# Performance work log

Hardware: AMD Instinct MI355X
Metric: run time of the kernel (lower is better)

The kernel has to match this reference:

```python
import jax, jax.numpy as jnp
import numpy as np

N_NODES = 100000


def _graph_conv(x, W, b, src, dst, n_nodes):
    # DGL GraphConv, norm='both':
    #   h = x * out_deg(src)^{-1/2}; h = h @ W; agg = scatter_sum over dst;
    #   out = agg * in_deg(dst)^{-1/2} + b
    ones = jnp.ones(src.shape, dtype=x.dtype)
    out_deg = jax.ops.segment_sum(ones, src, num_segments=n_nodes)
    in_deg = jax.ops.segment_sum(ones, dst, num_segments=n_nodes)
    norm_src = jax.lax.rsqrt(jnp.maximum(out_deg, 1.0))  # [N]
    norm_dst = jax.lax.rsqrt(jnp.maximum(in_deg, 1.0))   # [N]
    h = (x * norm_src[:, None]) @ W                      # [N, hid]
    msgs = h[src]                                        # [E, hid] gather
    agg = jax.ops.segment_sum(msgs, dst, num_segments=n_nodes)  # [N, hid]
    return jax.nn.relu(agg * norm_dst[:, None] + b)


def setup_inputs() -> dict:
    key = jax.random.key(0)
    k1, k2, k3, k4, k5 = jax.random.split(key, 5)
    n, e, d = N_NODES, 1600000, 128
    x = jax.random.normal(k1, (n, d), dtype=jnp.float32)
    src = jax.random.randint(k2, (e,), 0, n, dtype=jnp.int32)
    dst = jax.random.randint(k3, (e,), 0, n, dtype=jnp.int32)
    # Xavier-ish init for GraphConv weights, zero bias (DGL default)
    W1 = jax.random.normal(k4, (d, d), dtype=jnp.float32) / np.sqrt(d)
    W2 = jax.random.normal(k5, (d, d), dtype=jnp.float32) / np.sqrt(d)
    b1 = jnp.zeros((d,), dtype=jnp.float32)
    b2 = jnp.zeros((d,), dtype=jnp.float32)
    return {"x": x, "W1": W1, "b1": b1, "W2": W2, "b2": b2, "src": src, "dst": dst}


def reference(x, W1, b1, W2, b2, src, dst):
    h = _graph_conv(x, W1, b1, src, dst, N_NODES)
    h = _graph_conv(h, W2, b2, src, dst, N_NODES)
    return h
```

## Files before the change

kernel.cpp:

```cpp
#include <hip/hip_runtime.h>
#include <hip/hip_fp16.h>

#define HD 128
#define CHUNK 8192
#define MAXNB 512

typedef _Float16 f16x8 __attribute__((ext_vector_type(8)));
typedef float f32x4 __attribute__((ext_vector_type(4)));

__global__ __launch_bounds__(256) void hist_coarse(const int* __restrict__ dst,
                                                   unsigned int* __restrict__ gHist,
                                                   int NB, int NC, int E) {
    __shared__ unsigned int hist[MAXNB];
    for (int b = threadIdx.x; b < NB; b += 256) hist[b] = 0;
    __syncthreads();
    int base = blockIdx.x * CHUNK;
    int e0 = base + 4 * threadIdx.x;
#pragma unroll
    for (int it = 0; it < CHUNK / 1024; ++it, e0 += 1024) {
        if (e0 + 3 < E) {
            int4 d4 = *(const int4*)(dst + e0);
            atomicAdd(&hist[d4.x >> 8], 1u);
            atomicAdd(&hist[d4.y >> 8], 1u);
            atomicAdd(&hist[d4.z >> 8], 1u);
            atomicAdd(&hist[d4.w >> 8], 1u);
        } else {
            for (int j = 0; j < 4; ++j)
                if (e0 + j < E) atomicAdd(&hist[dst[e0 + j] >> 8], 1u);
        }
    }
    __syncthreads();
    for (int b = threadIdx.x; b < NB; b += 256)
        gHist[(size_t)b * NC + blockIdx.x] = hist[b];
}

__global__ __launch_bounds__(256) void make_norm_src(const unsigned int* __restrict__ cnt4s,
                                                     float* __restrict__ norm_src, int N) {
    int i = blockIdx.x * 256 + threadIdx.x;
    if (i < N) {
        float od = (float)(cnt4s[i] + cnt4s[N + i] + cnt4s[2 * N + i] + cnt4s[3 * N + i]);
        norm_src[i] = rsqrtf(od > 1.f ? od : 1.f);
    }
}

__global__ __launch_bounds__(256) void prep_w(const float* __restrict__ W1,
                                              const float* __restrict__ W2,
                                              _Float16* __restrict__ Wt) {
    const float* W = blockIdx.x ? W2 : W1;
    _Float16* T = Wt + (size_t)blockIdx.x * HD * HD;
    for (int i = threadIdx.x; i < HD * HD; i += 256) {
        int k = i >> 7, c = i & 127;
        T[c * HD + k] = (_Float16)W[i];
    }
}

__global__ __launch_bounds__(256) void scan_a(const unsigned int* __restrict__ cnt,
                                              unsigned int* __restrict__ excl,
                                              unsigned int* __restrict__ bsum, int n) {
    int i = blockIdx.x * 256 + threadIdx.x;
    unsigned int v = (i < n) ? cnt[i] : 0u;
    unsigned int x = v;
#pragma unroll
    for (int d = 1; d < 64; d <<= 1) {
        unsigned int y = __shfl_up(x, d, 64);
        if ((threadIdx.x & 63) >= d) x += y;
    }
    __shared__ unsigned int wsum[4];
    if ((threadIdx.x & 63) == 63) wsum[threadIdx.x >> 6] = x;
    __syncthreads();
    unsigned int woff = 0;
    for (int w = 0; w < (int)(threadIdx.x >> 6); ++w) woff += wsum[w];
    unsigned int incl = x + woff;
    if (i < n) excl[i] = incl - v;
    if (threadIdx.x == 255) bsum[blockIdx.x] = incl;
}

__global__ __launch_bounds__(1024) void scan_b(const unsigned int* __restrict__ bsum,
                                               unsigned int* __restrict__ boff, int nb) {
    int t = threadIdx.x;
    unsigned int v = (t < nb) ? bsum[t] : 0u;
    unsigned int x = v;
#pragma unroll
    for (int d = 1; d < 64; d <<= 1) {
        unsigned int y = __shfl_up(x, d, 64);
        if ((t & 63) >= d) x += y;
    }
    __shared__ unsigned int wsum[16];
    if ((t & 63) == 63) wsum[t >> 6] = x;
    __syncthreads();
    unsigned int woff = 0;
    for (int w = 0; w < (t >> 6); ++w) woff += wsum[w];
    unsigned int incl = x + woff;
    if (t < nb) boff[t] = incl - v;
}

__global__ __launch_bounds__(256) void scan_c(unsigned int* __restrict__ excl,
                                              const unsigned int* __restrict__ boff, int n) {
    int i = blockIdx.x * 256 + threadIdx.x;
    if (i < n) excl[i] += boff[blockIdx.x];
}

__global__ __launch_bounds__(256) void scatter_coarse(const int* __restrict__ src,
                                                      const int* __restrict__ dst,
                                                      const unsigned int* __restrict__ scanA,
                                                      unsigned int* __restrict__ packed,
                                                      unsigned int* __restrict__ cnt4s,
                                                      int N, int NB, int NC, int E) {
    __shared__ unsigned int curs[MAXNB];
    int chunk = blockIdx.x;
    for (int b = threadIdx.x; b < NB; b += 256)
        curs[b] = scanA[(size_t)b * NC + chunk];
    __syncthreads();
    int base = chunk * CHUNK;
    int e0 = base + 4 * threadIdx.x;
#pragma unroll
    for (int it = 0; it < CHUNK / 1024; ++it, e0 += 1024) {
        if (e0 + 3 < E) {
            int4 s4 = *(const int4*)(src + e0);
            int4 d4 = *(const int4*)(dst + e0);
            atomicAdd(&cnt4s[0 * N + s4.x], 1u);
            atomicAdd(&cnt4s[1 * N + s4.y], 1u);
            atomicAdd(&cnt4s[2 * N + s4.z], 1u);
            atomicAdd(&cnt4s[3 * N + s4.w], 1u);
            unsigned int p0 = atomicAdd(&curs[d4.x >> 8], 1u);
            unsigned int p1 = atomicAdd(&curs[d4.y >> 8], 1u);
            unsigned int p2 = atomicAdd(&curs[d4.z >> 8], 1u);
            unsigned int p3 = atomicAdd(&curs[d4.w >> 8], 1u);
            packed[p0] = ((unsigned int)(d4.x & 255) << 24) | (unsigned int)s4.x;
            packed[p1] = ((unsigned int)(d4.y & 255) << 24) | (unsigned int)s4.y;
            packed[p2] = ((unsigned int)(d4.z & 255) << 24) | (unsigned int)s4.z;
            packed[p3] = ((unsigned int)(d4.w & 255) << 24) | (unsigned int)s4.w;
        } else {
            for (int j = 0; j < 4; ++j)
                if (e0 + j < E) {
                    int d = dst[e0 + j], s = src[e0 + j];
                    atomicAdd(&cnt4s[j * N + s], 1u);
                    unsigned int pos = atomicAdd(&curs[d >> 8], 1u);
                    packed[pos] = ((unsigned int)(d & 255) << 24) | (unsigned int)s;
                }
        }
    }
}

__global__ __launch_bounds__(256) void fine_sort(const unsigned int* __restrict__ packed,
                                                 const unsigned int* __restrict__ scanA,
                                                 int* __restrict__ sorted_src,
                                                 unsigned int* __restrict__ offsets,
                                                 unsigned int* __restrict__ cntg,
                                                 float* __restrict__ normd,
                                                 int NB, int NC, int N, int E) {
    __shared__ unsigned int cnt[256];
    __shared__ unsigned int curs[256];
    __shared__ unsigned int wsum[4];
    int b = blockIdx.x;
    int t = threadIdx.x;
    unsigned int S = scanA[(size_t)b * NC];
    unsigned int T = (b + 1 < NB) ? scanA[(size_t)(b + 1) * NC] : (unsigned int)E;
    cnt[t] = 0;
    __syncthreads();
    for (unsigned int j = S + t; j < T; j += 256)
        atomicAdd(&cnt[packed[j] >> 24], 1u);
    __syncthreads();
    unsigned int v = cnt[t], x = v;
    int lane = t & 63;
#pragma unroll
    for (int d = 1; d < 64; d <<= 1) {
        unsigned int y = __shfl_up(x, d, 64);
        if (lane >= d) x += y;
    }
    if (lane == 63) wsum[t >> 6] = x;
    __syncthreads();
    unsigned int woff = 0;
    for (int w = 0; w < (t >> 6); ++w) woff += wsum[w];
    unsigned int ex = x - v + woff;
    curs[t] = ex;
    int node = b * 256 + t;
    if (node < N) {
        offsets[node] = S + ex;
        cntg[node] = v;
        float f = (float)v;
        normd[node] = rsqrtf(f > 1.f ? f : 1.f);
    }
    __syncthreads();
    for (unsigned int j = S + t; j < T; j += 256) {
        unsigned int p = packed[j];
        unsigned int pos = S + atomicAdd(&curs[p >> 24], 1u);
        sorted_src[pos] = (int)(p & 0xFFFFFFu);
    }
}

__global__ __launch_bounds__(256) void gemm_mfma_f32(const float* __restrict__ x,
                                                     const float* __restrict__ norm,
                                                     const _Float16* __restrict__ Wt,
                                                     _Float16* __restrict__ h, int n) {
    const int tid = threadIdx.x;
    const int w  = tid >> 6;
    const int l  = tid & 63;
    const int lg = l >> 4;
    const int li = l & 15;
    const int m  = blockIdx.x * 64 + w * 16 + li;

    f16x8 xf[4];
    if (m < n) {
        float nr = norm[m];
        const float* xrow = x + (size_t)m * HD + lg * 8;
#pragma unroll
        for (int kk = 0; kk < 4; ++kk) {
            float4 a = *(const float4*)(xrow + kk * 32);
            float4 b = *(const float4*)(xrow + kk * 32 + 4);
            f16x8 v;
            v[0] = (_Float16)(a.x * nr); v[1] = (_Float16)(a.y * nr);
            v[2] = (_Float16)(a.z * nr); v[3] = (_Float16)(a.w * nr);
            v[4] = (_Float16)(b.x * nr); v[5] = (_Float16)(b.y * nr);
            v[6] = (_Float16)(b.z * nr); v[7] = (_Float16)(b.w * nr);
            xf[kk] = v;
        }
    } else {
#pragma unroll
        for (int kk = 0; kk < 4; ++kk) xf[kk] = (f16x8){};
    }

    f32x4 acc[8];
#pragma unroll
    for (int t = 0; t < 8; ++t) acc[t] = (f32x4){0.f, 0.f, 0.f, 0.f};

#pragma unroll
    for (int t = 0; t < 8; ++t) {
        const _Float16* wrow = Wt + (size_t)(t * 16 + li) * HD + lg * 8;
#pragma unroll
        for (int kk = 0; kk < 4; ++kk) {
            f16x8 wf = *(const f16x8*)(wrow + kk * 32);
            acc[t] = __builtin_amdgcn_mfma_f32_16x16x32_f16(wf, xf[kk], acc[t], 0, 0, 0);
        }
    }

    if (m < n) {
        _Float16* hp = h + (size_t)m * HD + lg * 4;
#pragma unroll
        for (int t = 0; t < 8; ++t) {
            __half2 p0 = __floats2half2_rn(acc[t][0], acc[t][1]);
            __half2 p1 = __floats2half2_rn(acc[t][2], acc[t][3]);
            uint2 pk;
            pk.x = *(unsigned int*)&p0;
            pk.y = *(unsigned int*)&p1;
            *(uint2*)(hp + t * 16) = pk;
        }
    }
}

__global__ __launch_bounds__(256) void gemm_mfma(const _Float16* __restrict__ xh,
                                                 const _Float16* __restrict__ Wt,
                                                 _Float16* __restrict__ h, int n) {
    const int tid = threadIdx.x;
    const int w  = tid >> 6;
    const int l  = tid & 63;
    const int lg = l >> 4;
    const int li = l & 15;
    const int m  = blockIdx.x * 64 + w * 16 + li;

    const _Float16* xrow = xh + (size_t)m * HD + lg * 8;
    f16x8 xf[4];
#pragma unroll
    for (int kk = 0; kk < 4; ++kk)
        xf[kk] = *(const f16x8*)(xrow + kk * 32);

    f32x4 acc[8];
#pragma unroll
    for (int t = 0; t < 8; ++t) acc[t] = (f32x4){0.f, 0.f, 0.f, 0.f};

#pragma unroll
    for (int t = 0; t < 8; ++t) {
        const _Float16* wrow = Wt + (size_t)(t * 16 + li) * HD + lg * 8;
#pragma unroll
        for (int kk = 0; kk < 4; ++kk) {
            f16x8 wf = *(const f16x8*)(wrow + kk * 32);
            acc[t] = __builtin_amdgcn_mfma_f32_16x16x32_f16(wf, xf[kk], acc[t], 0, 0, 0);
        }
    }

    if (m < n) {
        _Float16* hp = h + (size_t)m * HD + lg * 4;
#pragma unroll
        for (int t = 0; t < 8; ++t) {
            __half2 p0 = __floats2half2_rn(acc[t][0], acc[t][1]);
            __half2 p1 = __floats2half2_rn(acc[t][2], acc[t][3]);
            uint2 pk;
            pk.x = *(unsigned int*)&p0;
            pk.y = *(unsigned int*)&p1;
            *(uint2*)(hp + t * 16) = pk;
        }
    }
}

template <bool MID>
__global__ __launch_bounds__(256) void aggregate_k(const __half* __restrict__ h,
                                                   const int* __restrict__ sorted_src,
                                                   const unsigned int* __restrict__ offsets,
                                                   const unsigned int* __restrict__ cnt,
                                                   const float* __restrict__ norm_dst,
                                                   const float* __restrict__ nsrc,
                                                   const float* __restrict__ bias,
                                                   float* __restrict__ outF,
                                                   __half* __restrict__ outH, int n) {
    int node = blockIdx.x * 4 + (int)(threadIdx.x >> 6);
    if (node >= n) return;
    int lane = threadIdx.x & 63;
    int g   = lane >> 4;
    int sub = lane & 15;

    unsigned int start = offsets[node];
    unsigned int deg   = cnt[node];
    const int* sp = sorted_src + start;
    const uint4* h4 = (const uint4*)h;

    float acc[8];
#pragma unroll
    for (int j = 0; j < 8; ++j) acc[j] = 0.f;

#define ACCUM(u)                                                                  \
    { float2 f;                                                                   \
      f = __half22float2(*(const __half2*)&(u).x); acc[0] += f.x; acc[1] += f.y;  \
      f = __half22float2(*(const __half2*)&(u).y); acc[2] += f.x; acc[3] += f.y;  \
      f = __half22float2(*(const __half2*)&(u).z); acc[4] += f.x; acc[5] += f.y;  \
      f = __half22float2(*(const __half2*)&(u).w); acc[6] += f.x; acc[7] += f.y; }

    unsigned int i = 0;
    for (; i + 16 <= deg; i += 16) {
        int s0 = sp[i + g];
        int s1 = sp[i + 4 + g];
        int s2 = sp[i + 8 + g];
        int s3 = sp[i + 12 + g];
        uint4 u0 = h4[(size_t)s0 * 16 + sub];
        uint4 u1 = h4[(size_t)s1 * 16 + sub];
        uint4 u2 = h4[(size_t)s2 * 16 + sub];
        uint4 u3 = h4[(size_t)s3 * 16 + sub];
        ACCUM(u0);
        ACCUM(u1);
        ACCUM(u2);
        ACCUM(u3);
    }
    for (; i < deg; i += 4) {
        if (i + g < deg) {
            int s = sp[i + g];
            uint4 u = h4[(size_t)s * 16 + sub];
            ACCUM(u);
        }
    }
#undef ACCUM

#pragma unroll
    for (int j = 0; j < 8; ++j) {
        acc[j] += __shfl_xor(acc[j], 16, 64);
        acc[j] += __shfl_xor(acc[j], 32, 64);
    }

    float nd = norm_dst[node];
    int col2 = sub * 4 + g;
    float2 bb = ((const float2*)bias)[col2];
    float vx = fmaxf(fmaf(acc[g * 2 + 0], nd, bb.x), 0.f);
    float vy = fmaxf(fmaf(acc[g * 2 + 1], nd, bb.y), 0.f);
    if (MID) {
        float ns = nsrc[node];
        __half2 p = __floats2half2_rn(vx * ns, vy * ns);
        ((__half2*)outH)[(size_t)node * 64 + col2] = p;
    } else {
        ((float2*)outF)[(size_t)node * 64 + col2] = make_float2(vx, vy);
    }
}

extern "C" void kernel_launch(void* const* d_in, const int* in_sizes, int n_in,
                              void* d_out, int out_size, void* d_ws, size_t ws_size,
                              hipStream_t stream) {
    const float* x   = (const float*)d_in[0];
    const float* W1  = (const float*)d_in[1];
    const float* b1  = (const float*)d_in[2];
    const float* W2  = (const float*)d_in[3];
    const float* b2  = (const float*)d_in[4];
    const int*   src = (const int*)d_in[5];
    const int*   dst = (const int*)d_in[6];

    const int N = in_sizes[0] / HD;
    const int E = in_sizes[5];
    float* out = (float*)d_out;

    const int NP = (N + 63) & ~63;
    const int NB = (N + 255) / 256;
    const int NC = (E + CHUNK - 1) / CHUNK;
    const int scanLen = NB * NC;
    const int nbS = (scanLen + 255) / 256;
    const int nbN = (N + 255) / 256;

    float*        norm_src = (float*)d_ws;
    float*        normd    = norm_src + N;
    unsigned int* cntg     = (unsigned int*)(normd + N);
    unsigned int* offsets  = cntg + N;
    unsigned int* cnt4s    = offsets + N;
    unsigned int* gHist    = cnt4s + 4 * N;
    unsigned int* scanA    = gHist + scanLen;
    unsigned int* bsum     = scanA + scanLen;
    unsigned int* boff     = bsum + 1024;
    unsigned int* packed   = boff + 1024;
    int*          sorted   = (int*)(packed + E);
    _Float16*     h        = (_Float16*)(sorted + E);
    _Float16*     xh       = h + (size_t)NP * HD;
    _Float16*     Wt       = xh + (size_t)NP * HD;

    hipMemsetAsync(cnt4s, 0, (size_t)4 * N * 4, stream);
    prep_w<<<2, 256, 0, stream>>>(W1, W2, Wt);
    hist_coarse<<<NC, 256, 0, stream>>>(dst, gHist, NB, NC, E);
    scan_a<<<nbS, 256, 0, stream>>>(gHist, scanA, bsum, scanLen);
    scan_b<<<1, 1024, 0, stream>>>(bsum, boff, nbS);
    scan_c<<<nbS, 256, 0, stream>>>(scanA, boff, scanLen);
    scatter_coarse<<<NC, 256, 0, stream>>>(src, dst, scanA, packed, cnt4s, N, NB, NC, E);
    make_norm_src<<<nbN, 256, 0, stream>>>(cnt4s, norm_src, N);
    fine_sort<<<NB, 256, 0, stream>>>(packed, scanA, sorted, offsets, cntg, normd, NB, NC, N, E);

    gemm_mfma_f32<<<NP / 64, 256, 0, stream>>>(x, norm_src, Wt, h, N);
    aggregate_k<true><<<(N + 3) / 4, 256, 0, stream>>>((const __half*)h, sorted, offsets, cntg,
                                                       normd, norm_src, b1, nullptr,
                                                       (__half*)xh, N);

    gemm_mfma<<<NP / 64, 256, 0, stream>>>(xh, Wt + HD * HD, h, N);
    aggregate_k<false><<<(N + 3) / 4, 256, 0, stream>>>((const __half*)h, sorted, offsets, cntg,
                                                        normd, nullptr, b2, out, nullptr, N);
}
```

Baseline: 352.0 us.

## Fold prep, scan fixup and norm kernels into neighbors; spread out-degree atomics

Merges the weight-transpose kernel into the coarse histogram launch as extra blocks, removes the scan_c fixup by adding block offsets on read in scatter and fine_sort, and computes norm_src inside fine_sort instead of a separate kernel. Out-degree counters are replicated eight ways instead of four to reduce global atomic contention. This cuts three kernel launches from the preprocessing chain. In exchange, the memset is larger and fine_sort must read eight count arrays.

```diff
diff --git a/kernel.cpp b/kernel.cpp
--- a/kernel.cpp
+++ b/kernel.cpp
@@ -8,9 +8,22 @@
 typedef _Float16 f16x8 __attribute__((ext_vector_type(8)));
 typedef float f32x4 __attribute__((ext_vector_type(4)));
 
-__global__ __launch_bounds__(256) void hist_coarse(const int* __restrict__ dst,
-                                                   unsigned int* __restrict__ gHist,
-                                                   int NB, int NC, int E) {
+__global__ __launch_bounds__(256) void hist_prep(const int* __restrict__ dst,
+                                                 unsigned int* __restrict__ gHist,
+                                                 const float* __restrict__ W1,
+                                                 const float* __restrict__ W2,
+                                                 _Float16* __restrict__ Wt,
+                                                 int NB, int NC, int E) {
+    if ((int)blockIdx.x >= NC) {
+        int which = blockIdx.x - NC;
+        const float* W = which ? W2 : W1;
+        _Float16* T = Wt + (size_t)which * HD * HD;
+        for (int i = threadIdx.x; i < HD * HD; i += 256) {
+            int k = i >> 7, c = i & 127;
+            T[c * HD + k] = (_Float16)W[i];
+        }
+        return;
+    }
     __shared__ unsigned int hist[MAXNB];
     for (int b = threadIdx.x; b < NB; b += 256) hist[b] = 0;
     __syncthreads();
@@ -34,26 +47,6 @@
         gHist[(size_t)b * NC + blockIdx.x] = hist[b];
 }
 
-__global__ __launch_bounds__(256) void make_norm_src(const unsigned int* __restrict__ cnt4s,
-                                                     float* __restrict__ norm_src, int N) {
-    int i = blockIdx.x * 256 + threadIdx.x;
-    if (i < N) {
-        float od = (float)(cnt4s[i] + cnt4s[N + i] + cnt4s[2 * N + i] + cnt4s[3 * N + i]);
-        norm_src[i] = rsqrtf(od > 1.f ? od : 1.f);
-    }
-}
-
-__global__ __launch_bounds__(256) void prep_w(const float* __restrict__ W1,
-                                              const float* __restrict__ W2,
-                                              _Float16* __restrict__ Wt) {
-    const float* W = blockIdx.x ? W2 : W1;
-    _Float16* T = Wt + (size_t)blockIdx.x * HD * HD;
-    for (int i = threadIdx.x; i < HD * HD; i += 256) {
-        int k = i >> 7, c = i & 127;
-        T[c * HD + k] = (_Float16)W[i];
-    }
-}
-
 __global__ __launch_bounds__(256) void scan_a(const unsigned int* __restrict__ cnt,
                                               unsigned int* __restrict__ excl,
                                               unsigned int* __restrict__ bsum, int n) {
@@ -94,34 +87,32 @@
     if (t < nb) boff[t] = incl - v;
 }
 
-__global__ __launch_bounds__(256) void scan_c(unsigned int* __restrict__ excl,
-                                              const unsigned int* __restrict__ boff, int n) {
-    int i = blockIdx.x * 256 + threadIdx.x;
-    if (i < n) excl[i] += boff[blockIdx.x];
-}
-
 __global__ __launch_bounds__(256) void scatter_coarse(const int* __restrict__ src,
                                                       const int* __restrict__ dst,
                                                       const unsigned int* __restrict__ scanA,
+                                                      const unsigned int* __restrict__ boff,
                                                       unsigned int* __restrict__ packed,
-                                                      unsigned int* __restrict__ cnt4s,
+                                                      unsigned int* __restrict__ cnt8s,
                                                       int N, int NB, int NC, int E) {
     __shared__ unsigned int curs[MAXNB];
     int chunk = blockIdx.x;
-    for (int b = threadIdx.x; b < NB; b += 256)
-        curs[b] = scanA[(size_t)b * NC + chunk];
+    for (int b = threadIdx.x; b < NB; b += 256) {
+        size_t idx = (size_t)b * NC + chunk;
+        curs[b] = scanA[idx] + boff[idx >> 8];
+    }
     __syncthreads();
     int base = chunk * CHUNK;
     int e0 = base + 4 * threadIdx.x;
+    const int rb = (threadIdx.x & 1) << 2;
 #pragma unroll
     for (int it = 0; it < CHUNK / 1024; ++it, e0 += 1024) {
         if (e0 + 3 < E) {
             int4 s4 = *(const int4*)(src + e0);
             int4 d4 = *(const int4*)(dst + e0);
-            atomicAdd(&cnt4s[0 * N + s4.x], 1u);
-            atomicAdd(&cnt4s[1 * N + s4.y], 1u);
-            atomicAdd(&cnt4s[2 * N + s4.z], 1u);
-            atomicAdd(&cnt4s[3 * N + s4.w], 1u);
+            atomicAdd(&cnt8s[(size_t)(rb + 0) * N + s4.x], 1u);
+            atomicAdd(&cnt8s[(size_t)(rb + 1) * N + s4.y], 1u);
+            atomicAdd(&cnt8s[(size_t)(rb + 2) * N + s4.z], 1u);
+            atomicAdd(&cnt8s[(size_t)(rb + 3) * N + s4.w], 1u);
             unsigned int p0 = atomicAdd(&curs[d4.x >> 8], 1u);
             unsigned int p1 = atomicAdd(&curs[d4.y >> 8], 1u);
             unsigned int p2 = atomicAdd(&curs[d4.z >> 8], 1u);
@@ -134,7 +125,7 @@
             for (int j = 0; j < 4; ++j)
                 if (e0 + j < E) {
                     int d = dst[e0 + j], s = src[e0 + j];
-                    atomicAdd(&cnt4s[j * N + s], 1u);
+                    atomicAdd(&cnt8s[(size_t)(rb + j) * N + s], 1u);
                     unsigned int pos = atomicAdd(&curs[d >> 8], 1u);
                     packed[pos] = ((unsigned int)(d & 255) << 24) | (unsigned int)s;
                 }
@@ -144,19 +135,38 @@
 
 __global__ __launch_bounds__(256) void fine_sort(const unsigned int* __restrict__ packed,
                                                  const unsigned int* __restrict__ scanA,
+                                                 const unsigned int* __restrict__ boff,
+                                                 const unsigned int* __restrict__ cnt8s,
                                                  int* __restrict__ sorted_src,
                                                  unsigned int* __restrict__ offsets,
                                                  unsigned int* __restrict__ cntg,
                                                  float* __restrict__ normd,
+                                                 float* __restrict__ norm_src,
                                                  int NB, int NC, int N, int E) {
     __shared__ unsigned int cnt[256];
     __shared__ unsigned int curs[256];
     __shared__ unsigned int wsum[4];
     int b = blockIdx.x;
     int t = threadIdx.x;
-    unsigned int S = scanA[(size_t)b * NC];
-    unsigned int T = (b + 1 < NB) ? scanA[(size_t)(b + 1) * NC] : (unsigned int)E;
+    size_t si = (size_t)b * NC;
+    unsigned int S = scanA[si] + boff[si >> 8];
+    unsigned int T;
+    if (b + 1 < NB) {
+        size_t ti = (size_t)(b + 1) * NC;
+        T = scanA[ti] + boff[ti >> 8];
+    } else {
+        T = (unsigned int)E;
+    }
     cnt[t] = 0;
+
+    int node = b * 256 + t;
+    if (node < N) {
+        unsigned int od = 0;
+#pragma unroll
+        for (int r = 0; r < 8; ++r) od += cnt8s[(size_t)r * N + node];
+        float f = (float)od;
+        norm_src[node] = rsqrtf(f > 1.f ? f : 1.f);
+    }
     __syncthreads();
     for (unsigned int j = S + t; j < T; j += 256)
         atomicAdd(&cnt[packed[j] >> 24], 1u);
@@ -174,7 +184,6 @@
     for (int w = 0; w < (t >> 6); ++w) woff += wsum[w];
     unsigned int ex = x - v + woff;
     curs[t] = ex;
-    int node = b * 256 + t;
     if (node < N) {
         offsets[node] = S + ex;
         cntg[node] = v;
@@ -388,14 +397,13 @@
     const int NC = (E + CHUNK - 1) / CHUNK;
     const int scanLen = NB * NC;
     const int nbS = (scanLen + 255) / 256;
-    const int nbN = (N + 255) / 256;
 
     float*        norm_src = (float*)d_ws;
     float*        normd    = norm_src + N;
     unsigned int* cntg     = (unsigned int*)(normd + N);
     unsigned int* offsets  = cntg + N;
-    unsigned int* cnt4s    = offsets + N;
-    unsigned int* gHist    = cnt4s + 4 * N;
+    unsigned int* cnt8s    = offsets + N;
+    unsigned int* gHist    = cnt8s + 8 * (size_t)N;
     unsigned int* scanA    = gHist + scanLen;
     unsigned int* bsum     = scanA + scanLen;
     unsigned int* boff     = bsum + 1024;
@@ -405,15 +413,13 @@
     _Float16*     xh       = h + (size_t)NP * HD;
     _Float16*     Wt       = xh + (size_t)NP * HD;
 
-    hipMemsetAsync(cnt4s, 0, (size_t)4 * N * 4, stream);
-    prep_w<<<2, 256, 0, stream>>>(W1, W2, Wt);
-    hist_coarse<<<NC, 256, 0, stream>>>(dst, gHist, NB, NC, E);
+    hipMemsetAsync(cnt8s, 0, (size_t)8 * N * 4, stream);
+    hist_prep<<<NC + 2, 256, 0, stream>>>(dst, gHist, W1, W2, Wt, NB, NC, E);
     scan_a<<<nbS, 256, 0, stream>>>(gHist, scanA, bsum, scanLen);
     scan_b<<<1, 1024, 0, stream>>>(bsum, boff, nbS);
-    scan_c<<<nbS, 256, 0, stream>>>(scanA, boff, scanLen);
-    scatter_coarse<<<NC, 256, 0, stream>>>(src, dst, scanA, packed, cnt4s, N, NB, NC, E);
-    make_norm_src<<<nbN, 256, 0, stream>>>(cnt4s, norm_src, N);
-    fine_sort<<<NB, 256, 0, stream>>>(packed, scanA, sorted, offsets, cntg, normd, NB, NC, N, E);
+    scatter_coarse<<<NC, 256, 0, stream>>>(src, dst, scanA, boff, packed, cnt8s, N, NB, NC, E);
+    fine_sort<<<NB, 256, 0, stream>>>(packed, scanA, boff, cnt8s, sorted, offsets, cntg,
+                                      normd, norm_src, NB, NC, N, E);
 
     gemm_mfma_f32<<<NP / 64, 256, 0, stream>>>(x, norm_src, Wt, h, N);
     aggregate_k<true><<<(N + 3) / 4, 256, 0, stream>>>((const __half*)h, sorted, offsets, cntg,
```

Measured after the change: 343.2 us. -2.5%, faster.
